# Kernel tuning notes

Hardware: AMD Instinct MI355X
Metric: run time of the kernel (lower is better)

Reference implementation:

```python
import jax, jax.numpy as jnp
import numpy as np

BN_EPS = 1e-5
KNN_K = 9
HEAD = 4


def _bn(x, gamma, beta, axis=1):
    # eval-mode BatchNorm with running_mean=0, running_var=1
    shape = [1] * x.ndim
    shape[axis] = -1
    scale = (gamma / jnp.sqrt(1.0 + BN_EPS)).reshape(shape)
    return x * scale + beta.reshape(shape)


def _conv1d(x, W, b):
    # 1x1 Conv1d == channel matmul; x: [B,C,N], W: [O,C], b: [O]
    return jnp.einsum('oc,bcn->bon', W, x) + b[None, :, None]


def _knn_idx(x, k):
    # x: [B,C,N] -> idx [B,N,k] of k nearest (incl. self)
    xx = jnp.sum(x * x, axis=1)                      # [B,N]
    inner = jnp.einsum('bcn,bcm->bnm', x, x)         # [B,N,N]
    neg_d = 2.0 * inner - xx[:, :, None] - xx[:, None, :]
    return jax.lax.top_k(neg_d, k)[1]


def _graph_feature(x, k):
    # x: [B,C,N] -> [B,2C,N,k]  (cat of center feature and center - neighbor)
    B, C, N = x.shape
    idx = _knn_idx(x, k)                             # [B,N,k]
    xt = jnp.transpose(x, (0, 2, 1))                 # [B,N,C]
    nbr = jax.vmap(lambda xb, ib: xb[ib])(xt, idx)   # [B,N,k,C]
    ctr = jnp.broadcast_to(xt[:, :, None, :], (B, N, k, C))
    feat = jnp.concatenate([ctr, ctr - nbr], axis=3)  # [B,N,k,2C]
    return jnp.transpose(feat, (0, 3, 1, 2))


def _dgcnn_max(x, w1, b1, g1, be1, w2, b2, g2, be2, k):
    # x: [B,C,N] -> [B,C,N]; two 1x1 convs + BN + ReLU then max over k
    ef = _graph_feature(x, k)                        # [B,2C,N,k]
    h = jnp.einsum('oc,bcnk->bonk', w1, ef) + b1[None, :, None, None]
    h = jax.nn.relu(_bn(h, g1, be1, axis=1))
    h = jnp.einsum('oc,bcnk->bonk', w2, h) + b2[None, :, None, None]
    h = jax.nn.relu(_bn(h, g2, be2, axis=1))
    return jnp.max(h, axis=-1)                       # [B,C,N]


def _attention(m1, m2, wq, bq, wk, bk, wv, bv, wmh, bmh, wc1, bc1, cg, cbe, wc2, bc2):
    B, C, N = m1.shape
    hd = C // HEAD
    q = _conv1d(m1, wq, bq).reshape(B, HEAD, hd, N)
    kk = _conv1d(m2, wk, bk).reshape(B, HEAD, hd, -1)
    v = _conv1d(m2, wv, bv).reshape(B, HEAD, hd, -1)
    score = jax.nn.softmax(jnp.einsum('bhdn,bhdm->bhnm', q, kk) / (float(hd) ** 0.5), axis=-1)
    add = jnp.einsum('bhnm,bhdm->bhdn', score, v).reshape(B, C, N)
    add = _conv1d(add, wmh, bmh)
    cat = jnp.concatenate([m1, add], axis=1)         # [B,2C,N]
    h = jax.nn.relu(_bn(_conv1d(cat, wc1, bc1), cg, cbe, axis=1))
    return m1 + _conv1d(h, wc2, bc2)


def setup_inputs() -> dict:
    key = jax.random.key(0)
    B, C, N = 4, 128, 2000
    ks = jax.random.split(key, 24)

    def w(k, shape, s=0.05):
        return jax.random.normal(k, shape, dtype=jnp.float32) * s

    inp = {
        'x': jax.random.normal(ks[0], (B, C, N, 1), dtype=jnp.float32),
        'y': jax.random.normal(ks[1], (B, C, N), dtype=jnp.float32),
        # DGCNN_MAX_Block conv params (two 1x1 Conv2d + BN)
        'dg_w1': w(ks[2], (C, 2 * C)), 'dg_b1': w(ks[3], (C,)),
        'dg_g1': jnp.ones((C,), jnp.float32), 'dg_be1': jnp.zeros((C,), jnp.float32),
        'dg_w2': w(ks[4], (C, C)), 'dg_b2': w(ks[5], (C,)),
        'dg_g2': jnp.ones((C,), jnp.float32), 'dg_be2': jnp.zeros((C,), jnp.float32),
        # AttentionPropagation params
        'wq': w(ks[6], (C, C)), 'bq': w(ks[7], (C,)),
        'wk': w(ks[8], (C, C)), 'bk': w(ks[9], (C,)),
        'wv': w(ks[10], (C, C)), 'bv': w(ks[11], (C,)),
        'wmh': w(ks[12], (C, C)), 'bmh': w(ks[13], (C,)),
        'wc1': w(ks[14], (2 * C, 2 * C)), 'bc1': w(ks[15], (2 * C,)),
        'cg': jnp.ones((2 * C,), jnp.float32), 'cbe': jnp.zeros((2 * C,), jnp.float32),
        'wc2': w(ks[16], (C, 2 * C)), 'bc2': w(ks[17], (C,)),
    }
    return inp


def reference(x, y, dg_w1, dg_b1, dg_g1, dg_be1, dg_w2, dg_b2, dg_g2, dg_be2,
              wq, bq, wk, bk, wv, bv, wmh, bmh, wc1, bc1, cg, cbe, wc2, bc2):
    feats = x[:, :, :, 0]                            # [B,C,N]
    agg = _dgcnn_max(feats, dg_w1, dg_b1, dg_g1, dg_be1,
                     dg_w2, dg_b2, dg_g2, dg_be2, KNN_K)
    out = _attention(agg, y, wq, bq, wk, bk, wv, bv, wmh, bmh,
                     wc1, bc1, cg, cbe, wc2, bc2)
    return out[:, :, :, None]                        # [B,C,N,1]
```

## Files before the change

kernel.cpp:

```cpp
#include <hip/hip_runtime.h>

#define BATCH 4
#define CH    128
#define NPTS  2000
#define KNN   9
#define NHEAD 4
#define HD    32

typedef unsigned short u16;
typedef __attribute__((ext_vector_type(4))) float f32x4;
typedef __attribute__((ext_vector_type(8))) short bf16x8;

#define OFF_XT    0
#define OFF_YT    1024000
#define OFF_PT    2048000
#define OFF_QT    3072000
#define OFF_AGG   4096000
#define OFF_MH    5120000
#define OFF_MISC  6144000
#define OFF_W1SUM (OFF_MISC)
#define OFF_W1B   (OFF_MISC+16384)
#define OFF_W2T   (OFF_MISC+32768)
#define OFF_WQT   (OFF_MISC+49152)
#define OFF_WKT   (OFF_MISC+65536)
#define OFF_WVT   (OFF_MISC+81920)
#define OFF_WMHT  (OFF_MISC+98304)
#define OFF_WC1T  (OFF_MISC+114688)
#define OFF_WC2T  (OFF_MISC+180224)
#define OFF_B1F   (OFF_MISC+212992)
#define OFF_B2F   (OFF_MISC+213120)
#define OFF_BC1F  (OFF_MISC+213248)
#define OFF_XX    (OFF_MISC+213504)
#define OFF_IDX   (OFF_MISC+221504)

__device__ __forceinline__ void bsplit(float v, u16& hi, u16& lo)
{
    unsigned u = __float_as_uint(v);
    unsigned h16 = (u + 0x7fffu + ((u >> 16) & 1u)) >> 16;
    float hf = __uint_as_float(h16 << 16);
    float lf = v - hf;
    unsigned ul = __float_as_uint(lf);
    hi = (u16)h16;
    lo = (u16)((ul + 0x7fffu + ((ul >> 16) & 1u)) >> 16);
}

__device__ __forceinline__ f32x4 mfma16(bf16x8 a, bf16x8 b, f32x4 c)
{
    return __builtin_amdgcn_mfma_f32_16x16x32_bf16(a, b, c, 0, 0, 0);
}

__global__ __launch_bounds__(256) void prep_kernel(
    const float* __restrict__ w1, const float* __restrict__ b1,
    const float* __restrict__ g1, const float* __restrict__ be1,
    const float* __restrict__ w2, const float* __restrict__ b2,
    const float* __restrict__ g2, const float* __restrict__ be2,
    const float* __restrict__ wq, const float* __restrict__ wk,
    const float* __restrict__ wv, const float* __restrict__ wmh,
    const float* __restrict__ wc1, const float* __restrict__ bc1,
    const float* __restrict__ cg, const float* __restrict__ cbe,
    const float* __restrict__ wc2, float* __restrict__ ws)
{
    int id = blockIdx.x * 256 + threadIdx.x;
    const float rs = rsqrtf(1.f + 1e-5f);
    if (id < 16384) {
        int c = id >> 7, o = id & 127;
        float s1 = g1[o] * rs;
        ws[OFF_W1SUM + id] = (w1[o*256 + c] + w1[o*256 + 128 + c]) * s1;
        ws[OFF_W1B   + id] = w1[o*256 + 128 + c] * s1;
        float s2 = g2[o] * rs;
        ws[OFF_W2T   + id] = w2[o*128 + c] * s2;
        ws[OFF_WQT   + id] = wq[o*128 + c];
        ws[OFF_WKT   + id] = wk[o*128 + c];
        ws[OFF_WVT   + id] = wv[o*128 + c];
        ws[OFF_WMHT  + id] = wmh[o*128 + c];
    }
    if (id < 32768) {
        int c = id >> 7, o = id & 127;
        ws[OFF_WC2T + id] = wc2[o*256 + c];
    }
    {
        int c = id >> 8, o = id & 255;
        ws[OFF_WC1T + id] = wc1[o*256 + c] * (cg[o] * rs);
    }
    if (id < 128) {
        float s1 = g1[id] * rs, s2 = g2[id] * rs;
        ws[OFF_B1F + id] = b1[id]*s1 + be1[id];
        ws[OFF_B2F + id] = b2[id]*s2 + be2[id];
    }
    if (id < 256) {
        ws[OFF_BC1F + id] = bc1[id]*(cg[id]*rs) + cbe[id];
    }
}

__global__ __launch_bounds__(128) void transpose_kernel(
    const float* __restrict__ src, float* __restrict__ dst, float* __restrict__ xx)
{
    int blk = blockIdx.x; int b = blk / NPTS, n = blk % NPTS;
    int c = threadIdx.x;
    float v = src[((size_t)b*CH + c)*NPTS + n];
    dst[((size_t)b*NPTS + n)*CH + c] = v;
    if (xx) {
        __shared__ float red[128];
        red[c] = v*v;
        __syncthreads();
        for (int s = 64; s > 0; s >>= 1) { if (c < s) red[c] += red[c+s]; __syncthreads(); }
        if (c == 0) xx[b*NPTS + n] = red[0];
    }
}

__global__ __launch_bounds__(256) void knn4_kernel(
    const u16* __restrict__ XH, const u16* __restrict__ XL,
    const float* __restrict__ xx, int* __restrict__ idxOut)
{
    __shared__ float woutv[4][16][9];
    __shared__ int   wouti[4][16][9];
    int b = blockIdx.y;
    int q0 = blockIdx.x * 16;
    int tid = threadIdx.x;
    int wave = tid >> 6, lane = tid & 63;
    int lg = lane >> 4, lr = lane & 15;
    const float* xxb = xx + (size_t)b*NPTS;

    size_t qb = ((size_t)b*NPTS + q0 + lr)*128 + lg*8;
    bf16x8 qh[4], ql[4];
#pragma unroll
    for (int ch = 0; ch < 4; ch++) {
        qh[ch] = *(const bf16x8*)&XH[qb + ch*32];
        ql[ch] = *(const bf16x8*)&XL[qb + ch*32];
    }

    float vals[4][9]; int ids[4][9];
    float vmin[4]; int amin[4];
#pragma unroll
    for (int j = 0; j < 4; j++) {
#pragma unroll
        for (int k = 0; k < 9; k++) { vals[j][k] = -3.4e38f; ids[j][k] = -1; }
        vmin[j] = -3.4e38f; amin[j] = 0;
    }

    for (int t = wave; t < 125; t += 4) {
        size_t kb = ((size_t)b*NPTS + t*16 + lr)*128 + lg*8;
        bf16x8 fh[4], fl[4];
#pragma unroll
        for (int ch = 0; ch < 4; ch++) {
            fh[ch] = *(const bf16x8*)&XH[kb + ch*32];
            fl[ch] = *(const bf16x8*)&XL[kb + ch*32];
        }
        float xv = xxb[t*16 + lr];
        f32x4 acc = {0.f,0.f,0.f,0.f};
#pragma unroll
        for (int ch = 0; ch < 4; ch++) {
            acc = mfma16(qh[ch], fh[ch], acc);
            acc = mfma16(qh[ch], fl[ch], acc);
            acc = mfma16(ql[ch], fh[ch], acc);
            acc = mfma16(ql[ch], fl[ch], acc);
        }
        int cand = t*16 + lr;
#pragma unroll
        for (int j = 0; j < 4; j++) {
            float s = 2.f*acc[j] - xv;
            if (s > vmin[j]) {
#pragma unroll
                for (int k = 0; k < 9; k++) {
                    bool sel = (k == amin[j]);
                    vals[j][k] = sel ? s    : vals[j][k];
                    ids[j][k]  = sel ? cand : ids[j][k];
                }
                vmin[j] = vals[j][0]; amin[j] = 0;
#pragma unroll
                for (int k = 1; k < 9; k++) {
                    bool lt = vals[j][k] < vmin[j];
                    vmin[j] = lt ? vals[j][k] : vmin[j];
                    amin[j] = lt ? k : amin[j];
                }
            }
        }
    }

#pragma unroll
    for (int j = 0; j < 4; j++) {
        unsigned used = 0;
        for (int r = 0; r < 9; r++) {
            float bv = -3.4e38f; int bm = -1;
#pragma unroll
            for (int k = 0; k < 9; k++) {
                bool ok = !(used & (1u << k)) && (vals[j][k] > bv);
                bv = ok ? vals[j][k] : bv;
                bm = ok ? ids[j][k]  : bm;
            }
            float v = bv; int mi = bm;
#pragma unroll
            for (int off = 1; off < 16; off <<= 1) {
                float ov = __shfl_xor(v, off);
                int  omi = __shfl_xor(mi, off);
                if (ov > v || (ov == v && omi >= 0 && omi < mi)) { v = ov; mi = omi; }
            }
#pragma unroll
            for (int k = 0; k < 9; k++) {
                if (ids[j][k] == mi) used |= (1u << k);
            }
            if (lr == 0) { woutv[wave][lg*4+j][r] = v; wouti[wave][lg*4+j][r] = mi; }
        }
    }
    __syncthreads();

    if (tid < 16) {
        float v0 = woutv[0][tid][0], v1 = woutv[1][tid][0], v2 = woutv[2][tid][0], v3 = woutv[3][tid][0];
        int   i0 = wouti[0][tid][0], i1 = wouti[1][tid][0], i2 = wouti[2][tid][0], i3 = wouti[3][tid][0];
        int   p0 = 1, p1 = 1, p2 = 1, p3 = 1;
        int* op = idxOut + ((size_t)b*NPTS + q0 + tid)*KNN;
        for (int r = 0; r < 9; r++) {
            int w = 0; float bv = v0; int bi = i0;
            if (v1 > bv || (v1 == bv && i1 < bi)) { w = 1; bv = v1; bi = i1; }
            if (v2 > bv || (v2 == bv && i2 < bi)) { w = 2; bv = v2; bi = i2; }
            if (v3 > bv || (v3 == bv && i3 < bi)) { w = 3; bv = v3; bi = i3; }
            op[r] = bi;
            if (w == 0)      { v0 = (p0 < 9) ? woutv[0][tid][p0] : -3.4e38f; i0 = (p0 < 9) ? wouti[0][tid][p0] : 0x7fffffff; p0++; }
            else if (w == 1) { v1 = (p1 < 9) ? woutv[1][tid][p1] : -3.4e38f; i1 = (p1 < 9) ? wouti[1][tid][p1] : 0x7fffffff; p1++; }
            else if (w == 2) { v2 = (p2 < 9) ? woutv[2][tid][p2] : -3.4e38f; i2 = (p2 < 9) ? wouti[2][tid][p2] : 0x7fffffff; p2++; }
            else             { v3 = (p3 < 9) ? woutv[3][tid][p3] : -3.4e38f; i3 = (p3 < 9) ? wouti[3][tid][p3] : 0x7fffffff; p3++; }
        }
    }
}

__global__ __launch_bounds__(128) void gemm_dual_kernel(
    const float* __restrict__ In, const float* __restrict__ Wa, const float* __restrict__ Wb,
    const float* __restrict__ ba, const float* __restrict__ bb,
    float* __restrict__ OutA, float* __restrict__ OutB)
{
    __shared__ float in_lds[8][128];
    int row0 = blockIdx.x * 8, tid = threadIdx.x;
    const float* src = In + (size_t)row0 * 128;
    for (int i = tid; i < 1024; i += 128) ((float*)in_lds)[i] = src[i];
    __syncthreads();
    float accA[8], accB[8];
    float bA = ba ? ba[tid] : 0.f, bB = bb ? bb[tid] : 0.f;
#pragma unroll
    for (int j = 0; j < 8; j++) { accA[j] = bA; accB[j] = bB; }
    for (int c = 0; c < 128; c++) {
        float wa = Wa[c*128 + tid], wb = Wb[c*128 + tid];
#pragma unroll
        for (int j = 0; j < 8; j++) {
            float x = in_lds[j][c];
            accA[j] += x * wa;
            accB[j] += x * wb;
        }
    }
#pragma unroll
    for (int j = 0; j < 8; j++) {
        OutA[(size_t)(row0 + j)*128 + tid] = accA[j];
        OutB[(size_t)(row0 + j)*128 + tid] = accB[j];
    }
}

template<int CIN, int COUT, bool RELU, bool TRANSOUT, bool HASRES, bool CONCAT>
__global__ __launch_bounds__(COUT) void gemmT_kernel(
    const float* __restrict__ In, const float* __restrict__ In2,
    const float* __restrict__ Wt, const float* __restrict__ bias,
    const float* __restrict__ Res, float* __restrict__ Out)
{
    __shared__ float in_lds[8][CIN];
    int row0 = blockIdx.x * 8, tid = threadIdx.x;
    if (!CONCAT) {
        const float* src = In + (size_t)row0 * CIN;
        for (int i = tid; i < 8*CIN; i += COUT) ((float*)in_lds)[i] = src[i];
    } else {
        for (int i = tid; i < 8*128; i += COUT) {
            int j = i >> 7, c = i & 127;
            in_lds[j][c]       = In [(size_t)(row0 + j)*128 + c];
            in_lds[j][128 + c] = In2[(size_t)(row0 + j)*128 + c];
        }
    }
    __syncthreads();
    float acc[8];
    float b = bias ? bias[tid] : 0.f;
#pragma unroll
    for (int j = 0; j < 8; j++) acc[j] = b;
    for (int c = 0; c < CIN; c++) {
        float w = Wt[c*COUT + tid];
#pragma unroll
        for (int j = 0; j < 8; j++) acc[j] += in_lds[j][c] * w;
    }
#pragma unroll
    for (int j = 0; j < 8; j++) {
        float v = acc[j];
        if (RELU) v = fmaxf(v, 0.f);
        size_t row = row0 + j;
        if (HASRES) v += Res[row*COUT + tid];
        if (!TRANSOUT) {
            Out[row*COUT + tid] = v;
        } else {
            int b_ = (int)(row / NPTS), n_ = (int)(row % NPTS);
            Out[((size_t)b_*COUT + tid)*NPTS + n_] = v;
        }
    }
}

__global__ __launch_bounds__(128) void edgeconv_kernel(
    const float* __restrict__ Pt, const float* __restrict__ Qt,
    const int* __restrict__ idx, const float* __restrict__ W2t,
    const float* __restrict__ b2f, float* __restrict__ Agg)
{
    int blk = blockIdx.x; int b = blk / NPTS, n = blk % NPTS;
    int o = threadIdx.x;
    __shared__ float r[128*9];
    __shared__ int mk[9];
    if (o < 9) mk[o] = idx[((size_t)b*NPTS + n)*KNN + o];
    __syncthreads();
    float p = Pt[((size_t)b*NPTS + n)*128 + o];
#pragma unroll
    for (int k = 0; k < 9; k++) {
        float q = Qt[((size_t)b*NPTS + mk[k])*128 + o];
        r[o*9 + k] = fmaxf(p - q, 0.f);
    }
    __syncthreads();
    float acc[9];
#pragma unroll
    for (int k = 0; k < 9; k++) acc[k] = 0.f;
    for (int c = 0; c < 128; c++) {
        float w = W2t[c*128 + o];
#pragma unroll
        for (int k = 0; k < 9; k++) acc[k] += r[c*9 + k] * w;
    }
    float bb = b2f[o];
    float vmax = -3.4e38f;
#pragma unroll
    for (int k = 0; k < 9; k++) vmax = fmaxf(vmax, fmaxf(acc[k] + bb, 0.f));
    Agg[((size_t)b*NPTS + n)*128 + o] = vmax;
}

__global__ __launch_bounds__(256) void split_bf16_kernel(
    const float* __restrict__ src, u16* __restrict__ H, u16* __restrict__ L)
{
    int id = blockIdx.x * 256 + threadIdx.x;
    float v = src[id];
    u16 hi, lo;
    bsplit(v, hi, lo);
    H[id] = hi; L[id] = lo;
}

__global__ __launch_bounds__(256) void split_v_kernel(
    const float* __restrict__ VA, u16* __restrict__ VTH, u16* __restrict__ VTL)
{
    __shared__ float t[32][33];
    int b = blockIdx.z, c0 = blockIdx.y * 32, n0 = blockIdx.x * 32;
    int tid = threadIdx.x;
    int cc = tid & 31, rr = tid >> 5;
#pragma unroll
    for (int p = 0; p < 4; p++) {
        int n = n0 + rr + p*8;
        t[rr + p*8][cc] = (n < NPTS) ? VA[((size_t)b*NPTS + n)*128 + c0 + cc] : 0.f;
    }
    __syncthreads();
#pragma unroll
    for (int p = 0; p < 4; p++) {
        int c = c0 + rr + p*8;
        int n = n0 + cc;
        if (n < NPTS) {
            u16 hi, lo;
            bsplit(t[cc][rr + p*8], hi, lo);
            size_t o = ((size_t)b*128 + c)*NPTS + n;
            VTH[o] = hi; VTL[o] = lo;
        }
    }
}

#define PSTR 72
__global__ __launch_bounds__(256) void attn_mfma_kernel(
    const u16* __restrict__ QH, const u16* __restrict__ QL,
    const u16* __restrict__ KH, const u16* __restrict__ KL,
    const u16* __restrict__ VTH, const u16* __restrict__ VTL,
    float* __restrict__ Add)
{
    __shared__ alignas(16) u16 Ph[4][16][PSTR];
    __shared__ alignas(16) u16 Pl[4][16][PSTR];
    int b = blockIdx.z, h = blockIdx.y;
    int wave = threadIdx.x >> 6, lane = threadIdx.x & 63;
    int lg = lane >> 4, lr = lane & 15;
    int q0 = blockIdx.x * 64 + wave * 16;
    if (q0 >= NPTS) return;

    size_t qb = ((size_t)b*NPTS + q0 + lr)*128 + h*32 + lg*8;
    const bf16x8 qh = *(const bf16x8*)&QH[qb];
    const bf16x8 ql = *(const bf16x8*)&QL[qb];

    f32x4 o0 = {0.f,0.f,0.f,0.f}, o1 = {0.f,0.f,0.f,0.f};
    float mrun[4], lsum[4];
#pragma unroll
    for (int r = 0; r < 4; r++) { mrun[r] = -3.0e38f; lsum[r] = 0.f; }
    const float sc = 0.17677669529663687f;
    int shsrc = ((lr >> 2) << 4) | (lr & 3);

    for (int ks = 0; ks < NPTS; ks += 32) {
        int r1 = ks + 16 + lr; if (r1 > NPTS-1) r1 = NPTS-1;
        size_t kb0 = ((size_t)b*NPTS + ks + lr)*128 + h*32 + lg*8;
        size_t kb1 = ((size_t)b*NPTS + r1)*128 + h*32 + lg*8;
        bf16x8 k0h = *(const bf16x8*)&KH[kb0];
        bf16x8 k0l = *(const bf16x8*)&KL[kb0];
        bf16x8 k1h = *(const bf16x8*)&KH[kb1];
        bf16x8 k1l = *(const bf16x8*)&KL[kb1];
        f32x4 s0 = {0.f,0.f,0.f,0.f}, s1 = {0.f,0.f,0.f,0.f};
        s0 = mfma16(qh, k0h, s0);
        s0 = mfma16(qh, k0l, s0);
        s0 = mfma16(ql, k0h, s0);
        s1 = mfma16(qh, k1h, s1);
        s1 = mfma16(qh, k1l, s1);
        s1 = mfma16(ql, k1h, s1);
        bool vk1 = (ks + 16 + lr) < NPTS;
        float mx[4];
#pragma unroll
        for (int r = 0; r < 4; r++) {
            float a  = s0[r]*sc;
            float a2 = vk1 ? s1[r]*sc : -3.0e38f;
            s0[r] = a; s1[r] = a2;
            mx[r] = fmaxf(a, a2);
        }
#pragma unroll
        for (int off = 1; off < 16; off <<= 1) {
#pragma unroll
            for (int r = 0; r < 4; r++) mx[r] = fmaxf(mx[r], __shfl_xor(mx[r], off));
        }
        float e0[4], e1[4], rsu[4], sca[4];
#pragma unroll
        for (int r = 0; r < 4; r++) {
            float mn = fmaxf(mrun[r], mx[r]);
            sca[r] = __expf(mrun[r] - mn);
            mrun[r] = mn;
            e0[r] = __expf(s0[r] - mn);
            e1[r] = __expf(s1[r] - mn);
            rsu[r] = e0[r] + e1[r];
        }
#pragma unroll
        for (int off = 1; off < 16; off <<= 1) {
#pragma unroll
            for (int r = 0; r < 4; r++) rsu[r] += __shfl_xor(rsu[r], off);
        }
#pragma unroll
        for (int r = 0; r < 4; r++) lsum[r] = lsum[r]*sca[r] + rsu[r];
#pragma unroll
        for (int r = 0; r < 4; r++) {
            u16 h0, w0, h1, w1;
            bsplit(e0[r], h0, w0);
            bsplit(e1[r], h1, w1);
            int qr = lg*4 + r;
            Ph[wave][qr][lr]      = h0;
            Pl[wave][qr][lr]      = w0;
            Ph[wave][qr][16 + lr] = h1;
            Pl[wave][qr][16 + lr] = w1;
        }
        float scsel = (lr & 2) ? ((lr & 1) ? sca[3] : sca[2])
                               : ((lr & 1) ? sca[1] : sca[0]);
        float osc = __shfl(scsel, shsrc);
#pragma unroll
        for (int r = 0; r < 4; r++) { o0[r] *= osc; o1[r] *= osc; }
        int cb = ks + lg*8; if (cb > NPTS-8) cb = NPTS-8;
        bf16x8 pbh = *(const bf16x8*)&Ph[wave][lr][lg*8];
        bf16x8 pbl = *(const bf16x8*)&Pl[wave][lr][lg*8];
        size_t vb = ((size_t)b*128 + h*32 + lr)*NPTS + cb;
        bf16x8 v0h = *(const bf16x8*)&VTH[vb];
        bf16x8 v0l = *(const bf16x8*)&VTL[vb];
        bf16x8 v1h = *(const bf16x8*)&VTH[vb + 16*NPTS];
        bf16x8 v1l = *(const bf16x8*)&VTL[vb + 16*NPTS];
        o0 = mfma16(v0h, pbh, o0);
        o0 = mfma16(v0l, pbh, o0);
        o0 = mfma16(v0h, pbl, o0);
        o1 = mfma16(v1h, pbh, o1);
        o1 = mfma16(v1l, pbh, o1);
        o1 = mfma16(v1h, pbl, o1);
    }
    float lsel = (lr & 2) ? ((lr & 1) ? lsum[3] : lsum[2])
                          : ((lr & 1) ? lsum[1] : lsum[0]);
    float rinv = 1.f / __shfl(lsel, shsrc);
    int q = q0 + lr;
    size_t ob = ((size_t)b*NPTS + q)*128 + h*32;
#pragma unroll
    for (int r = 0; r < 4; r++) {
        Add[ob + lg*4 + r]      = o0[r]*rinv;
        Add[ob + 16 + lg*4 + r] = o1[r]*rinv;
    }
}

extern "C" void kernel_launch(void* const* d_in, const int* in_sizes, int n_in,
                              void* d_out, int out_size, void* d_ws, size_t ws_size,
                              hipStream_t stream)
{
    const float* x    = (const float*)d_in[0];
    const float* y    = (const float*)d_in[1];
    const float* w1   = (const float*)d_in[2];
    const float* b1   = (const float*)d_in[3];
    const float* g1   = (const float*)d_in[4];
    const float* be1  = (const float*)d_in[5];
    const float* w2   = (const float*)d_in[6];
    const float* b2   = (const float*)d_in[7];
    const float* g2   = (const float*)d_in[8];
    const float* be2  = (const float*)d_in[9];
    const float* wq   = (const float*)d_in[10];
    const float* bq   = (const float*)d_in[11];
    const float* wk   = (const float*)d_in[12];
    const float* bk   = (const float*)d_in[13];
    const float* wv   = (const float*)d_in[14];
    const float* bv   = (const float*)d_in[15];
    const float* wmh  = (const float*)d_in[16];
    const float* bmh  = (const float*)d_in[17];
    const float* wc1  = (const float*)d_in[18];
    const float* bc1  = (const float*)d_in[19];
    const float* cg   = (const float*)d_in[20];
    const float* cbe  = (const float*)d_in[21];
    const float* wc2  = (const float*)d_in[22];
    const float* bc2  = (const float*)d_in[23];
    float* ws = (float*)d_ws;
    float* out = (float*)d_out;

    float* XT  = ws + OFF_XT;
    float* YT  = ws + OFF_YT;
    float* PT  = ws + OFF_PT;
    float* QT  = ws + OFF_QT;
    float* AGG = ws + OFF_AGG;
    float* MH  = ws + OFF_MH;
    float* XX  = ws + OFF_XX;
    int*   IDX = (int*)(ws + OFF_IDX);
    float* QA  = PT;
    float* KA  = PT;
    float* VA  = XT;
    float* ADD = YT;
    float* TT  = PT;
    const int SPE = BATCH*NPTS*CH;
    u16* XHs = (u16*)MH;  u16* XLs = XHs + SPE;
    u16* QHs = (u16*)MH;  u16* QLs = QHs + SPE;
    u16* KHs = (u16*)QT;  u16* KLs = KHs + SPE;
    u16* VTH = (u16*)PT;  u16* VTL = VTH + SPE;

    prep_kernel<<<256, 256, 0, stream>>>(w1, b1, g1, be1, w2, b2, g2, be2,
                                         wq, wk, wv, wmh, wc1, bc1, cg, cbe, wc2, ws);
    transpose_kernel<<<BATCH*NPTS, 128, 0, stream>>>(x, XT, XX);
    transpose_kernel<<<BATCH*NPTS, 128, 0, stream>>>(y, YT, nullptr);
    split_bf16_kernel<<<SPE/256, 256, 0, stream>>>(XT, XHs, XLs);
    knn4_kernel<<<dim3(NPTS/16, BATCH), 256, 0, stream>>>(XHs, XLs, XX, IDX);
    gemm_dual_kernel<<<BATCH*NPTS/8, 128, 0, stream>>>(XT, ws + OFF_W1SUM, ws + OFF_W1B,
                                                       ws + OFF_B1F, nullptr, PT, QT);
    edgeconv_kernel<<<BATCH*NPTS, 128, 0, stream>>>(PT, QT, IDX, ws + OFF_W2T,
                                                    ws + OFF_B2F, AGG);
    gemmT_kernel<128,128,false,false,false,false><<<BATCH*NPTS/8, 128, 0, stream>>>(
        AGG, nullptr, ws + OFF_WQT, bq, nullptr, QA);
    split_bf16_kernel<<<SPE/256, 256, 0, stream>>>(QA, QHs, QLs);
    gemm_dual_kernel<<<BATCH*NPTS/8, 128, 0, stream>>>(YT, ws + OFF_WKT, ws + OFF_WVT,
                                                       bk, bv, KA, VA);
    split_bf16_kernel<<<SPE/256, 256, 0, stream>>>(KA, KHs, KLs);
    split_v_kernel<<<dim3(63, 128/32, BATCH), 256, 0, stream>>>(VA, VTH, VTL);
    attn_mfma_kernel<<<dim3(32, NHEAD, BATCH), 256, 0, stream>>>(
        QHs, QLs, KHs, KLs, VTH, VTL, ADD);
    gemmT_kernel<128,128,false,false,false,false><<<BATCH*NPTS/8, 128, 0, stream>>>(
        ADD, nullptr, ws + OFF_WMHT, bmh, nullptr, MH);
    gemmT_kernel<256,256,true,false,false,true><<<BATCH*NPTS/8, 256, 0, stream>>>(
        AGG, MH, ws + OFF_WC1T, ws + OFF_BC1F, nullptr, TT);
    gemmT_kernel<256,128,false,true,true,false><<<BATCH*NPTS/8, 128, 0, stream>>>(
        TT, nullptr, ws + OFF_WC2T, bc2, AGG, out);
}
```

Before: 567.3 us.

## Use row-major weights with float4 dot loops, widen KNN to 8 waves, drop P low split

The 1x1-conv GEMM and edgeconv kernels now read each output's weight row as contiguous float4 and take vectorised dot products against the LDS inputs. This lets several weight transposes in prep be dropped, so raw wq/wk/wv/wmh/wc2 are passed straight through. The KNN kernel moves from 4 to 8 waves per block, splitting the candidate scan further and merging 8 partial top-9 lists. Attention now rounds the softmax probabilities to a single bf16 instead of a hi/lo pair, removing one MFMA per tile at some cost in accuracy. Per-thread row reads of weights are strided across threads, which may coalesce poorly compared with the old column layout.

After: 582.0 us. +2.6%, slower.

```diff
diff --git a/kernel.cpp b/kernel.cpp
--- a/kernel.cpp
+++ b/kernel.cpp
@@ -21,18 +21,18 @@
 #define OFF_W1SUM (OFF_MISC)
 #define OFF_W1B   (OFF_MISC+16384)
 #define OFF_W2T   (OFF_MISC+32768)
-#define OFF_WQT   (OFF_MISC+49152)
-#define OFF_WKT   (OFF_MISC+65536)
-#define OFF_WVT   (OFF_MISC+81920)
-#define OFF_WMHT  (OFF_MISC+98304)
 #define OFF_WC1T  (OFF_MISC+114688)
-#define OFF_WC2T  (OFF_MISC+180224)
 #define OFF_B1F   (OFF_MISC+212992)
 #define OFF_B2F   (OFF_MISC+213120)
 #define OFF_BC1F  (OFF_MISC+213248)
 #define OFF_XX    (OFF_MISC+213504)
 #define OFF_IDX   (OFF_MISC+221504)
 
+__device__ __forceinline__ u16 bf16rne(float v)
+{
+    unsigned u = __float_as_uint(v);
+    return (u16)((u + 0x7fffu + ((u >> 16) & 1u)) >> 16);
+}
 __device__ __forceinline__ void bsplit(float v, u16& hi, u16& lo)
 {
     unsigned u = __float_as_uint(v);
@@ -54,33 +54,22 @@
     const float* __restrict__ g1, const float* __restrict__ be1,
     const float* __restrict__ w2, const float* __restrict__ b2,
     const float* __restrict__ g2, const float* __restrict__ be2,
-    const float* __restrict__ wq, const float* __restrict__ wk,
-    const float* __restrict__ wv, const float* __restrict__ wmh,
     const float* __restrict__ wc1, const float* __restrict__ bc1,
     const float* __restrict__ cg, const float* __restrict__ cbe,
-    const float* __restrict__ wc2, float* __restrict__ ws)
+    float* __restrict__ ws)
 {
     int id = blockIdx.x * 256 + threadIdx.x;
     const float rs = rsqrtf(1.f + 1e-5f);
     if (id < 16384) {
-        int c = id >> 7, o = id & 127;
+        int o = id >> 7, c = id & 127;
         float s1 = g1[o] * rs;
         ws[OFF_W1SUM + id] = (w1[o*256 + c] + w1[o*256 + 128 + c]) * s1;
         ws[OFF_W1B   + id] = w1[o*256 + 128 + c] * s1;
-        float s2 = g2[o] * rs;
-        ws[OFF_W2T   + id] = w2[o*128 + c] * s2;
-        ws[OFF_WQT   + id] = wq[o*128 + c];
-        ws[OFF_WKT   + id] = wk[o*128 + c];
-        ws[OFF_WVT   + id] = wv[o*128 + c];
-        ws[OFF_WMHT  + id] = wmh[o*128 + c];
-    }
-    if (id < 32768) {
-        int c = id >> 7, o = id & 127;
-        ws[OFF_WC2T + id] = wc2[o*256 + c];
+        ws[OFF_W2T   + id] = w2[id] * (g2[o] * rs);
     }
     {
-        int c = id >> 8, o = id & 255;
-        ws[OFF_WC1T + id] = wc1[o*256 + c] * (cg[o] * rs);
+        int o = id >> 8;
+        ws[OFF_WC1T + id] = wc1[id] * (cg[o] * rs);
     }
     if (id < 128) {
         float s1 = g1[id] * rs, s2 = g2[id] * rs;
@@ -108,12 +97,12 @@
     }
 }
 
-__global__ __launch_bounds__(256) void knn4_kernel(
+__global__ __launch_bounds__(512) void knn8_kernel(
     const u16* __restrict__ XH, const u16* __restrict__ XL,
     const float* __restrict__ xx, int* __restrict__ idxOut)
 {
-    __shared__ float woutv[4][16][9];
-    __shared__ int   wouti[4][16][9];
+    __shared__ float woutv[8][16][9];
+    __shared__ int   wouti[8][16][9];
     int b = blockIdx.y;
     int q0 = blockIdx.x * 16;
     int tid = threadIdx.x;
@@ -138,7 +127,7 @@
         vmin[j] = -3.4e38f; amin[j] = 0;
     }
 
-    for (int t = wave; t < 125; t += 4) {
+    for (int t = wave; t < 125; t += 8) {
         size_t kb = ((size_t)b*NPTS + t*16 + lr)*128 + lg*8;
         bf16x8 fh[4], fl[4];
 #pragma unroll
@@ -206,19 +195,29 @@
 
     if (tid < 16) {
         float v0 = woutv[0][tid][0], v1 = woutv[1][tid][0], v2 = woutv[2][tid][0], v3 = woutv[3][tid][0];
+        float v4 = woutv[4][tid][0], v5 = woutv[5][tid][0], v6 = woutv[6][tid][0], v7 = woutv[7][tid][0];
         int   i0 = wouti[0][tid][0], i1 = wouti[1][tid][0], i2 = wouti[2][tid][0], i3 = wouti[3][tid][0];
-        int   p0 = 1, p1 = 1, p2 = 1, p3 = 1;
+        int   i4 = wouti[4][tid][0], i5 = wouti[5][tid][0], i6 = wouti[6][tid][0], i7 = wouti[7][tid][0];
+        int   p0 = 1, p1 = 1, p2 = 1, p3 = 1, p4 = 1, p5 = 1, p6 = 1, p7 = 1;
         int* op = idxOut + ((size_t)b*NPTS + q0 + tid)*KNN;
         for (int r = 0; r < 9; r++) {
             int w = 0; float bv = v0; int bi = i0;
             if (v1 > bv || (v1 == bv && i1 < bi)) { w = 1; bv = v1; bi = i1; }
             if (v2 > bv || (v2 == bv && i2 < bi)) { w = 2; bv = v2; bi = i2; }
             if (v3 > bv || (v3 == bv && i3 < bi)) { w = 3; bv = v3; bi = i3; }
+            if (v4 > bv || (v4 == bv && i4 < bi)) { w = 4; bv = v4; bi = i4; }
+            if (v5 > bv || (v5 == bv && i5 < bi)) { w = 5; bv = v5; bi = i5; }
+            if (v6 > bv || (v6 == bv && i6 < bi)) { w = 6; bv = v6; bi = i6; }
+            if (v7 > bv || (v7 == bv && i7 < bi)) { w = 7; bv = v7; bi = i7; }
             op[r] = bi;
             if (w == 0)      { v0 = (p0 < 9) ? woutv[0][tid][p0] : -3.4e38f; i0 = (p0 < 9) ? wouti[0][tid][p0] : 0x7fffffff; p0++; }
             else if (w == 1) { v1 = (p1 < 9) ? woutv[1][tid][p1] : -3.4e38f; i1 = (p1 < 9) ? wouti[1][tid][p1] : 0x7fffffff; p1++; }
             else if (w == 2) { v2 = (p2 < 9) ? woutv[2][tid][p2] : -3.4e38f; i2 = (p2 < 9) ? wouti[2][tid][p2] : 0x7fffffff; p2++; }
-            else             { v3 = (p3 < 9) ? woutv[3][tid][p3] : -3.4e38f; i3 = (p3 < 9) ? wouti[3][tid][p3] : 0x7fffffff; p3++; }
+            else if (w == 3) { v3 = (p3 < 9) ? woutv[3][tid][p3] : -3.4e38f; i3 = (p3 < 9) ? wouti[3][tid][p3] : 0x7fffffff; p3++; }
+            else if (w == 4) { v4 = (p4 < 9) ? woutv[4][tid][p4] : -3.4e38f; i4 = (p4 < 9) ? wouti[4][tid][p4] : 0x7fffffff; p4++; }
+            else if (w == 5) { v5 = (p5 < 9) ? woutv[5][tid][p5] : -3.4e38f; i5 = (p5 < 9) ? wouti[5][tid][p5] : 0x7fffffff; p5++; }
+            else if (w == 6) { v6 = (p6 < 9) ? woutv[6][tid][p6] : -3.4e38f; i6 = (p6 < 9) ? wouti[6][tid][p6] : 0x7fffffff; p6++; }
+            else             { v7 = (p7 < 9) ? woutv[7][tid][p7] : -3.4e38f; i7 = (p7 < 9) ? wouti[7][tid][p7] : 0x7fffffff; p7++; }
         }
     }
 }
@@ -237,13 +236,16 @@
     float bA = ba ? ba[tid] : 0.f, bB = bb ? bb[tid] : 0.f;
 #pragma unroll
     for (int j = 0; j < 8; j++) { accA[j] = bA; accB[j] = bB; }
-    for (int c = 0; c < 128; c++) {
-        float wa = Wa[c*128 + tid], wb = Wb[c*128 + tid];
+    const float4* wra = (const float4*)(Wa + (size_t)tid * 128);
+    const float4* wrb = (const float4*)(Wb + (size_t)tid * 128);
+#pragma unroll 4
+    for (int c4 = 0; c4 < 32; c4++) {
+        float4 wa = wra[c4], wb = wrb[c4];
 #pragma unroll
         for (int j = 0; j < 8; j++) {
-            float x = in_lds[j][c];
-            accA[j] += x * wa;
-            accB[j] += x * wb;
+            float4 xi = ((const float4*)&in_lds[j][0])[c4];
+            accA[j] += xi.x*wa.x + xi.y*wa.y + xi.z*wa.z + xi.w*wa.w;
+            accB[j] += xi.x*wb.x + xi.y*wb.y + xi.z*wb.z + xi.w*wb.w;
         }
     }
 #pragma unroll
@@ -276,10 +278,15 @@
     float b = bias ? bias[tid] : 0.f;
 #pragma unroll
     for (int j = 0; j < 8; j++) acc[j] = b;
-    for (int c = 0; c < CIN; c++) {
-        float w = Wt[c*COUT + tid];
-#pragma unroll
-        for (int j = 0; j < 8; j++) acc[j] += in_lds[j][c] * w;
+    const float4* wrow = (const float4*)(Wt + (size_t)tid * CIN);
+#pragma unroll 4
+    for (int c4 = 0; c4 < CIN/4; c4++) {
+        float4 w = wrow[c4];
+#pragma unroll
+        for (int j = 0; j < 8; j++) {
+            float4 xi = ((const float4*)&in_lds[j][0])[c4];
+            acc[j] += xi.x*w.x + xi.y*w.y + xi.z*w.z + xi.w*w.w;
+        }
     }
 #pragma unroll
     for (int j = 0; j < 8; j++) {
@@ -303,7 +310,7 @@
 {
     int blk = blockIdx.x; int b = blk / NPTS, n = blk % NPTS;
     int o = threadIdx.x;
-    __shared__ float r[128*9];
+    __shared__ float r[9][128];
     __shared__ int mk[9];
     if (o < 9) mk[o] = idx[((size_t)b*NPTS + n)*KNN + o];
     __syncthreads();
@@ -311,16 +318,21 @@
 #pragma unroll
     for (int k = 0; k < 9; k++) {
         float q = Qt[((size_t)b*NPTS + mk[k])*128 + o];
-        r[o*9 + k] = fmaxf(p - q, 0.f);
+        r[k][o] = fmaxf(p - q, 0.f);
     }
     __syncthreads();
     float acc[9];
 #pragma unroll
     for (int k = 0; k < 9; k++) acc[k] = 0.f;
-    for (int c = 0; c < 128; c++) {
-        float w = W2t[c*128 + o];
-#pragma unroll
-        for (int k = 0; k < 9; k++) acc[k] += r[c*9 + k] * w;
+    const float4* w2row = (const float4*)(W2t + (size_t)o * 128);
+#pragma unroll 2
+    for (int c4 = 0; c4 < 32; c4++) {
+        float4 w = w2row[c4];
+#pragma unroll
+        for (int k = 0; k < 9; k++) {
+            float4 rv = ((const float4*)&r[k][0])[c4];
+            acc[k] += rv.x*w.x + rv.y*w.y + rv.z*w.z + rv.w*w.w;
+        }
     }
     float bb = b2f[o];
     float vmax = -3.4e38f;
@@ -373,7 +385,6 @@
     float* __restrict__ Add)
 {
     __shared__ alignas(16) u16 Ph[4][16][PSTR];
-    __shared__ alignas(16) u16 Pl[4][16][PSTR];
     int b = blockIdx.z, h = blockIdx.y;
     int wave = threadIdx.x >> 6, lane = threadIdx.x & 63;
     int lg = lane >> 4, lr = lane & 15;
@@ -439,14 +450,9 @@
         for (int r = 0; r < 4; r++) lsum[r] = lsum[r]*sca[r] + rsu[r];
 #pragma unroll
         for (int r = 0; r < 4; r++) {
-            u16 h0, w0, h1, w1;
-            bsplit(e0[r], h0, w0);
-            bsplit(e1[r], h1, w1);
             int qr = lg*4 + r;
-            Ph[wave][qr][lr]      = h0;
-            Pl[wave][qr][lr]      = w0;
-            Ph[wave][qr][16 + lr] = h1;
-            Pl[wave][qr][16 + lr] = w1;
+            Ph[wave][qr][lr]      = bf16rne(e0[r]);
+            Ph[wave][qr][16 + lr] = bf16rne(e1[r]);
         }
         float scsel = (lr & 2) ? ((lr & 1) ? sca[3] : sca[2])
                                : ((lr & 1) ? sca[1] : sca[0]);
@@ -455,7 +461,6 @@
         for (int r = 0; r < 4; r++) { o0[r] *= osc; o1[r] *= osc; }
         int cb = ks + lg*8; if (cb > NPTS-8) cb = NPTS-8;
         bf16x8 pbh = *(const bf16x8*)&Ph[wave][lr][lg*8];
-        bf16x8 pbl = *(const bf16x8*)&Pl[wave][lr][lg*8];
         size_t vb = ((size_t)b*128 + h*32 + lr)*NPTS + cb;
         bf16x8 v0h = *(const bf16x8*)&VTH[vb];
         bf16x8 v0l = *(const bf16x8*)&VTL[vb];
@@ -463,10 +468,8 @@
         bf16x8 v1l = *(const bf16x8*)&VTL[vb + 16*NPTS];
         o0 = mfma16(v0h, pbh, o0);
         o0 = mfma16(v0l, pbh, o0);
-        o0 = mfma16(v0h, pbl, o0);
         o1 = mfma16(v1h, pbh, o1);
         o1 = mfma16(v1l, pbh, o1);
-        o1 = mfma16(v1h, pbl, o1);
     }
     float lsel = (lr & 2) ? ((lr & 1) ? lsum[3] : lsum[2])
                           : ((lr & 1) ? lsum[1] : lsum[0]);
@@ -531,28 +534,27 @@
     u16* VTH = (u16*)PT;  u16* VTL = VTH + SPE;
 
     prep_kernel<<<256, 256, 0, stream>>>(w1, b1, g1, be1, w2, b2, g2, be2,
-                                         wq, wk, wv, wmh, wc1, bc1, cg, cbe, wc2, ws);
+                                         wc1, bc1, cg, cbe, ws);
     transpose_kernel<<<BATCH*NPTS, 128, 0, stream>>>(x, XT, XX);
     transpose_kernel<<<BATCH*NPTS, 128, 0, stream>>>(y, YT, nullptr);
     split_bf16_kernel<<<SPE/256, 256, 0, stream>>>(XT, XHs, XLs);
-    knn4_kernel<<<dim3(NPTS/16, BATCH), 256, 0, stream>>>(XHs, XLs, XX, IDX);
+    knn8_kernel<<<dim3(NPTS/16, BATCH), 512, 0, stream>>>(XHs, XLs, XX, IDX);
     gemm_dual_kernel<<<BATCH*NPTS/8, 128, 0, stream>>>(XT, ws + OFF_W1SUM, ws + OFF_W1B,
                                                        ws + OFF_B1F, nullptr, PT, QT);
     edgeconv_kernel<<<BATCH*NPTS, 128, 0, stream>>>(PT, QT, IDX, ws + OFF_W2T,
                                                     ws + OFF_B2F, AGG);
     gemmT_kernel<128,128,false,false,false,false><<<BATCH*NPTS/8, 128, 0, stream>>>(
-        AGG, nullptr, ws + OFF_WQT, bq, nullptr, QA);
+        AGG, nullptr, wq, bq, nullptr, QA);
     split_bf16_kernel<<<SPE/256, 256, 0, stream>>>(QA, QHs, QLs);
-    gemm_dual_kernel<<<BATCH*NPTS/8, 128, 0, stream>>>(YT, ws + OFF_WKT, ws + OFF_WVT,
-                                                       bk, bv, KA, VA);
+    gemm_dual_kernel<<<BATCH*NPTS/8, 128, 0, stream>>>(YT, wk, wv, bk, bv, KA, VA);
     split_bf16_kernel<<<SPE/256, 256, 0, stream>>>(KA, KHs, KLs);
     split_v_kernel<<<dim3(63, 128/32, BATCH), 256, 0, stream>>>(VA, VTH, VTL);
     attn_mfma_kernel<<<dim3(32, NHEAD, BATCH), 256, 0, stream>>>(
         QHs, QLs, KHs, KLs, VTH, VTL, ADD);
     gemmT_kernel<128,128,false,false,false,false><<<BATCH*NPTS/8, 128, 0, stream>>>(
-        ADD, nullptr, ws + OFF_WMHT, bmh, nullptr, MH);
+        ADD, nullptr, wmh, bmh, nullptr, MH);
     gemmT_kernel<256,256,true,false,false,true><<<BATCH*NPTS/8, 256, 0, stream>>>(
         AGG, MH, ws + OFF_WC1T, ws + OFF_BC1F, nullptr, TT);
     gemmT_kernel<256,128,false,true,true,false><<<BATCH*NPTS/8, 128, 0, stream>>>(
-        TT, nullptr, ws + OFF_WC2T, bc2, AGG, out);
-}
+        TT, nullptr, wc2, bc2, AGG, out);
+}
```
